# Performance work log

Hardware: AMD Instinct MI355X
Metric: run time of the kernel (lower is better)

The kernel has to match this reference:

```python
import jax, jax.numpy as jnp
import numpy as np

EOS_IDX = 2


def setup_inputs() -> dict:
    key = jax.random.key(0)
    k1, k2 = jax.random.split(key)
    B, S, D = 64, 2048, 1024
    feature = jax.random.normal(k1, (B, S, D), dtype=jnp.float32)
    input_ids = jax.random.randint(k2, (B, S), 3, 33, dtype=jnp.int64)
    # guarantee every row has an eos (last column), like real tokenized sequences
    input_ids = input_ids.at[:, S - 1].set(EOS_IDX)
    return {"feature": feature, "input_ids": input_ids}


def reference(feature, input_ids):
    # MEAN pooling: for each row i, mean over feature[i, 1:last_eos_i, :]
    B, S, D = feature.shape
    pos = jnp.arange(S)
    eq = input_ids == EOS_IDX                       # [B, S]
    # last eos position; 0 if none (matches torch zeros init)
    last_eos = jnp.max(jnp.where(eq, pos[None, :], 0), axis=1)  # [B]
    # mask positions j with 1 <= j < last_eos_i
    mask = ((pos[None, :] >= 1) & (pos[None, :] < last_eos[:, None])).astype(feature.dtype)  # [B, S]
    summed = jnp.einsum("bsd,bs->bd", feature, mask)            # [B, D]
    counts = jnp.sum(mask, axis=1, keepdims=True)               # [B, 1]
    return summed / counts
```

## Files before the change

### kernel.cpp

```cpp
#include <hip/hip_runtime.h>

#define EOS_IDX 2
#define NSPLIT 16

typedef float v4f __attribute__((ext_vector_type(4)));

__device__ __forceinline__ int row_last_eos(const int* __restrict__ row, int S) {
    int m = 0;
    for (int j = threadIdx.x; j < S; j += blockDim.x) {
        if (row[j] == EOS_IDX) m = max(m, j);
    }
    #pragma unroll
    for (int off = 32; off > 0; off >>= 1) m = max(m, __shfl_xor(m, off, 64));
    __shared__ int sm[8];
    const int wid = threadIdx.x >> 6;
    const int nw  = blockDim.x >> 6;
    if ((threadIdx.x & 63) == 0) sm[wid] = m;
    __syncthreads();
    int r = sm[0];
    for (int w = 1; w < nw; ++w) r = max(r, sm[w]);
    return r;
}

__global__ __launch_bounds__(256) void pool_kernel(const float* __restrict__ feat,
                                                   const int* __restrict__ ids,
                                                   float* __restrict__ partial,
                                                   int S, int D, int jchunk) {
    const int b  = blockIdx.x;
    const int le = row_last_eos(ids + (size_t)b * S, S);
    const float inv = 1.0f / (float)(le - 1);

    const int j0 = blockIdx.y * jchunk;
    const int lo = max(j0, 1);
    const int hi = min(j0 + jchunk, le);

    const int d4n = D >> 2;
    const v4f* base = (const v4f*)(feat + (size_t)b * S * D);
    v4f* pout = (v4f*)(partial + ((size_t)b * NSPLIT + blockIdx.y) * D);

    for (int d4 = threadIdx.x; d4 < d4n; d4 += blockDim.x) {
        v4f s0 = {0.f, 0.f, 0.f, 0.f};
        v4f s1 = s0, s2 = s0, s3 = s0, s4 = s0, s5 = s0, s6 = s0, s7 = s0;
        int j = lo;
        for (; j + 8 <= hi; j += 8) {
            const v4f* p = base + (size_t)j * d4n + d4;
            v4f a0 = __builtin_nontemporal_load(p + 0 * d4n);
            v4f a1 = __builtin_nontemporal_load(p + 1 * d4n);
            v4f a2 = __builtin_nontemporal_load(p + 2 * d4n);
            v4f a3 = __builtin_nontemporal_load(p + 3 * d4n);
            v4f a4 = __builtin_nontemporal_load(p + 4 * d4n);
            v4f a5 = __builtin_nontemporal_load(p + 5 * d4n);
            v4f a6 = __builtin_nontemporal_load(p + 6 * d4n);
            v4f a7 = __builtin_nontemporal_load(p + 7 * d4n);
            s0 += a0; s1 += a1; s2 += a2; s3 += a3;
            s4 += a4; s5 += a5; s6 += a6; s7 += a7;
        }
        for (; j < hi; ++j)
            s0 += __builtin_nontemporal_load(base + (size_t)j * d4n + d4);
        v4f t = ((s0 + s1) + (s2 + s3)) + ((s4 + s5) + (s6 + s7));
        pout[d4] = t * inv;
    }
}

__global__ __launch_bounds__(256) void reduce_kernel(const float* __restrict__ partial,
                                                     float* __restrict__ out, int D) {
    const int b   = blockIdx.x;
    const int d4n = D >> 2;
    const v4f* p  = (const v4f*)(partial + (size_t)b * NSPLIT * D);
    v4f* o        = (v4f*)(out + (size_t)b * D);
    for (int d4 = threadIdx.x; d4 < d4n; d4 += blockDim.x) {
        v4f s = {0.f, 0.f, 0.f, 0.f};
        #pragma unroll
        for (int t = 0; t < NSPLIT; ++t) s += p[(size_t)t * d4n + d4];
        o[d4] = s;
    }
}

extern "C" void kernel_launch(void* const* d_in, const int* in_sizes, int n_in,
                              void* d_out, int out_size, void* d_ws, size_t ws_size,
                              hipStream_t stream) {
    const float* feat = (const float*)d_in[0];
    const int*   ids  = (const int*)d_in[1];

    const int BS = in_sizes[1];
    const int D  = in_sizes[0] / BS;
    const int B  = out_size / D;
    const int S  = BS / B;

    float* partial = (float*)d_ws;

    const int jchunk = (S + NSPLIT - 1) / NSPLIT;
    dim3 pgrid(B, NSPLIT);
    pool_kernel<<<pgrid, 256, 0, stream>>>(feat, ids, partial, S, D, jchunk);

    reduce_kernel<<<B, 256, 0, stream>>>(partial, (float*)d_out, D);
}
```

Measured before the change: 89.60 us.

## Fuse pool and reduce into one cooperative kernel with grid sync

```diff
diff --git a/kernel.cpp b/kernel.cpp
--- a/kernel.cpp
+++ b/kernel.cpp
@@ -1,7 +1,10 @@
 #include <hip/hip_runtime.h>
+#include <hip/hip_cooperative_groups.h>
+
+namespace cg = cooperative_groups;
 
 #define EOS_IDX 2
-#define NSPLIT 16
+#define NSPLIT 8
 
 typedef float v4f __attribute__((ext_vector_type(4)));
 
@@ -22,10 +25,10 @@
     return r;
 }
 
-__global__ __launch_bounds__(256) void pool_kernel(const float* __restrict__ feat,
-                                                   const int* __restrict__ ids,
-                                                   float* __restrict__ partial,
-                                                   int S, int D, int jchunk) {
+__device__ __forceinline__ void pool_body(const float* __restrict__ feat,
+                                          const int* __restrict__ ids,
+                                          float* __restrict__ partial,
+                                          int S, int D, int jchunk) {
     const int b  = blockIdx.x;
     const int le = row_last_eos(ids + (size_t)b * S, S);
     const float inv = 1.0f / (float)(le - 1);
@@ -62,8 +65,8 @@
     }
 }
 
-__global__ __launch_bounds__(256) void reduce_kernel(const float* __restrict__ partial,
-                                                     float* __restrict__ out, int D) {
+__device__ __forceinline__ void reduce_body(const float* __restrict__ partial,
+                                            float* __restrict__ out, int D) {
     const int b   = blockIdx.x;
     const int d4n = D >> 2;
     const v4f* p  = (const v4f*)(partial + (size_t)b * NSPLIT * D);
@@ -76,6 +79,29 @@
     }
 }
 
+__global__ __launch_bounds__(256) void fused_kernel(const float* __restrict__ feat,
+                                                    const int* __restrict__ ids,
+                                                    float* __restrict__ partial,
+                                                    float* __restrict__ out,
+                                                    int S, int D, int jchunk) {
+    pool_body(feat, ids, partial, S, D, jchunk);
+    __threadfence();
+    cg::this_grid().sync();
+    if (blockIdx.y == 0) reduce_body(partial, out, D);
+}
+
+__global__ __launch_bounds__(256) void pool_kernel(const float* __restrict__ feat,
+                                                   const int* __restrict__ ids,
+                                                   float* __restrict__ partial,
+                                                   int S, int D, int jchunk) {
+    pool_body(feat, ids, partial, S, D, jchunk);
+}
+
+__global__ __launch_bounds__(256) void reduce_kernel(const float* __restrict__ partial,
+                                                     float* __restrict__ out, int D) {
+    reduce_body(partial, out, D);
+}
+
 extern "C" void kernel_launch(void* const* d_in, const int* in_sizes, int n_in,
                               void* d_out, int out_size, void* d_ws, size_t ws_size,
                               hipStream_t stream) {
@@ -83,15 +109,23 @@
     const int*   ids  = (const int*)d_in[1];
 
     const int BS = in_sizes[1];
-    const int D  = in_sizes[0] / BS;
-    const int B  = out_size / D;
-    const int S  = BS / B;
+    int D = in_sizes[0] / BS;
+    const int B = out_size / D;
+    int S = BS / B;
 
     float* partial = (float*)d_ws;
+    float* out = (float*)d_out;
 
-    const int jchunk = (S + NSPLIT - 1) / NSPLIT;
-    dim3 pgrid(B, NSPLIT);
-    pool_kernel<<<pgrid, 256, 0, stream>>>(feat, ids, partial, S, D, jchunk);
+    int jchunk = (S + NSPLIT - 1) / NSPLIT;
+    dim3 grid(B, NSPLIT);
+    dim3 block(256);
 
-    reduce_kernel<<<B, 256, 0, stream>>>(partial, (float*)d_out, D);
+    void* args[] = {(void*)&feat, (void*)&ids, (void*)&partial, (void*)&out,
+                    (void*)&S, (void*)&D, (void*)&jchunk};
+    hipError_t err = hipLaunchCooperativeKernel((const void*)fused_kernel,
+                                                grid, block, args, 0, stream);
+    if (err != hipSuccess) {
+        pool_kernel<<<grid, block, 0, stream>>>(feat, ids, partial, S, D, jchunk);
+        reduce_kernel<<<B, block, 0, stream>>>(partial, out, D);
+    }
 }
```

Measured after the change: 212.8 us. 2.38x slower.
